# Kernel tuning notes

Hardware: AMD Instinct MI355X
Metric: run time of the kernel (lower is better)

## Reference

```python
import jax, jax.numpy as jnp
import numpy as np

SEQ, BATCH, D_IN, D_LAT = 512, 64, 1024, 1024

def setup_inputs() -> dict:
    key = jax.random.key(0)
    ks = jax.random.split(key, 5)
    scale = 0.02
    d_cat = D_IN + D_LAT
    return {
        "x":   jax.random.normal(ks[0], (SEQ, BATCH, D_IN), dtype=jnp.float32),
        "W_f": jax.random.normal(ks[1], (D_LAT, d_cat), dtype=jnp.float32) * scale,
        "b_f": jnp.zeros((D_LAT,), dtype=jnp.float32),
        "W_i": jax.random.normal(ks[2], (D_LAT, d_cat), dtype=jnp.float32) * scale,
        "b_i": jnp.zeros((D_LAT,), dtype=jnp.float32),
        "W_o": jax.random.normal(ks[3], (D_LAT, d_cat), dtype=jnp.float32) * scale,
        "b_o": jnp.zeros((D_LAT,), dtype=jnp.float32),
        "W_c": jax.random.normal(ks[4], (D_LAT, d_cat), dtype=jnp.float32) * scale,
        "b_c": jnp.zeros((D_LAT,), dtype=jnp.float32),
    }

def reference(x, W_f, b_f, W_i, b_i, W_o, b_o, W_c, b_c):
    # Fuse the 4 gate projections into one GEMM per step (same math).
    d_lat = W_f.shape[0]
    W_all = jnp.concatenate([W_f, W_i, W_o, W_c], axis=0)   # [4*d_lat, d_cat]
    b_all = jnp.concatenate([b_f, b_i, b_o, b_c], axis=0)   # [4*d_lat]
    batch = x.shape[1]
    h0 = jnp.zeros((batch, d_lat), dtype=x.dtype)
    c0 = jnp.zeros((batch, d_lat), dtype=x.dtype)

    def step(carry, x_t):
        h, c = carry
        z = jnp.concatenate([h, x_t], axis=-1)               # [batch, d_lat+d_in]
        gates = z @ W_all.T + b_all                          # [batch, 4*d_lat]
        f_t = jax.nn.sigmoid(gates[:, 0*d_lat:1*d_lat])
        i_t = jax.nn.sigmoid(gates[:, 1*d_lat:2*d_lat])
        o_t = jax.nn.sigmoid(gates[:, 2*d_lat:3*d_lat])
        g_t = jnp.tanh(gates[:, 3*d_lat:4*d_lat])
        c_t = f_t * c + i_t * g_t
        h_t = o_t * jnp.tanh(c_t)
        return (h_t, c_t), h_t

    _, hidden_states = jax.lax.scan(step, (h0, c0), x)       # [seq, batch, d_lat]
    return hidden_states
```

## Files before the change

### kernel.cpp

```cpp
#include <hip/hip_runtime.h>

#define SEQ   512
#define BATCH 64
#define D_IN  1024
#define D_LAT 1024
#define D_CAT 2048
#define NBLK  128
#define JPB   8
#define ROWS  32
#define THREADS 512
#define GPS   67

typedef unsigned short u16;
typedef __attribute__((ext_vector_type(8))) short short8;
typedef __attribute__((ext_vector_type(4))) float floatx4;

__device__ __forceinline__ u16 f2bf(float f) {
    union { float f; unsigned u; } a; a.f = f;
    unsigned u = a.u;
    return (u16)((u + 0x7FFFu + ((u >> 16) & 1u)) >> 16);
}

__device__ __forceinline__ float sigm(float x)  { return 1.0f / (1.0f + __expf(-x)); }
__device__ __forceinline__ float tanhf_(float x){ return 2.0f / (1.0f + __expf(-2.0f * x)) - 1.0f; }

__global__ void cvt_bf16(const float* __restrict__ x, u16* __restrict__ xb, int n8) {
    int i = blockIdx.x * blockDim.x + threadIdx.x;
    int stride = gridDim.x * blockDim.x;
    for (; i < n8; i += stride) {
        float4 v0 = ((const float4*)x)[2 * i];
        float4 v1 = ((const float4*)x)[2 * i + 1];
        short8 o;
        o[0] = (short)f2bf(v0.x); o[1] = (short)f2bf(v0.y);
        o[2] = (short)f2bf(v0.z); o[3] = (short)f2bf(v0.w);
        o[4] = (short)f2bf(v1.x); o[5] = (short)f2bf(v1.y);
        o[6] = (short)f2bf(v1.z); o[7] = (short)f2bf(v1.w);
        *(short8*)(xb + 8 * (size_t)i) = o;
    }
}


__launch_bounds__(THREADS, 1)
__global__ void lstm_persist(const float* __restrict__ Wf, const float* __restrict__ bfp,
                             const float* __restrict__ Wi, const float* __restrict__ bip,
                             const float* __restrict__ Wo, const float* __restrict__ bop,
                             const float* __restrict__ Wc, const float* __restrict__ bcp,
                             const u16* __restrict__ xb,
                             u16* __restrict__ hhist,
                             float* __restrict__ out,
                             unsigned* __restrict__ bar) {
    __shared__ __align__(16) float gp[8][ROWS][GPS];
    __shared__ float biasL[ROWS];

    const int tid  = threadIdx.x;
    const int jblk = blockIdx.x;
    const int c    = tid >> 6;
    const int lane = tid & 63;
    const int m    = lane & 15;
    const int q    = lane >> 4;
    const int grp  = jblk & 7;

    short8 bregH[2][4], bregX[2][4];
    #pragma unroll
    for (int rt = 0; rt < 2; ++rt) {
        const int rr  = rt * 16 + m;
        const int g   = rr >> 3;
        const int jj2 = rr & 7;
        const float* Wg = (g == 0) ? Wf : (g == 1) ? Wi : (g == 2) ? Wo : Wc;
        const float* rowp = Wg + (size_t)(jblk * JPB + jj2) * D_CAT;
        #pragma unroll
        for (int ks = 0; ks < 4; ++ks) {
            const float* ph = rowp + c * 128 + ks * 32 + q * 8;
            const float* px = rowp + 1024 + c * 128 + ks * 32 + q * 8;
            float4 h0 = *(const float4*)(ph);
            float4 h1 = *(const float4*)(ph + 4);
            float4 x0 = *(const float4*)(px);
            float4 x1 = *(const float4*)(px + 4);
            short8 bh, bx;
            bh[0] = (short)f2bf(h0.x); bh[1] = (short)f2bf(h0.y);
            bh[2] = (short)f2bf(h0.z); bh[3] = (short)f2bf(h0.w);
            bh[4] = (short)f2bf(h1.x); bh[5] = (short)f2bf(h1.y);
            bh[6] = (short)f2bf(h1.z); bh[7] = (short)f2bf(h1.w);
            bx[0] = (short)f2bf(x0.x); bx[1] = (short)f2bf(x0.y);
            bx[2] = (short)f2bf(x0.z); bx[3] = (short)f2bf(x0.w);
            bx[4] = (short)f2bf(x1.x); bx[5] = (short)f2bf(x1.y);
            bx[6] = (short)f2bf(x1.z); bx[7] = (short)f2bf(x1.w);
            bregH[rt][ks] = bh;
            bregX[rt][ks] = bx;
        }
    }
    if (tid < ROWS) {
        const float* bsrc = (tid < 8) ? bfp : (tid < 16) ? bip : (tid < 24) ? bop : bcp;
        biasL[tid] = bsrc[jblk * JPB + (tid & 7)];
    }
    __syncthreads();

    const int cb = tid >> 2;
    const int ca = tid & 3;
    float creg0 = 0.0f, creg1 = 0.0f;

    const int colbase = c * 128 + q * 8;

    #pragma unroll 1
    for (int t = 0; t < SEQ; ++t) {
        const u16* xptr = xb + (size_t)t * (BATCH * D_IN) + colbase;

        floatx4 acc[2][4];
        #pragma unroll
        for (int rt = 0; rt < 2; ++rt)
            #pragma unroll
            for (int bt = 0; bt < 4; ++bt)
                acc[rt][bt] = (floatx4){0.f, 0.f, 0.f, 0.f};

        #pragma unroll
        for (int ks = 0; ks < 4; ++ks) {
            #pragma unroll
            for (int bt = 0; bt < 4; ++bt) {
                short8 a = *(const short8*)(xptr + (size_t)(bt * 16 + m) * 1024 + ks * 32);
                acc[0][bt] = __builtin_amdgcn_mfma_f32_16x16x32_bf16(a, bregX[0][ks], acc[0][bt], 0, 0, 0);
                acc[1][bt] = __builtin_amdgcn_mfma_f32_16x16x32_bf16(a, bregX[1][ks], acc[1][bt], 0, 0, 0);
            }
        }

        asm volatile("" ::: "memory");
        if (tid == 0) {
            while (__hip_atomic_load(&bar[16], __ATOMIC_RELAXED,
                                     __HIP_MEMORY_SCOPE_AGENT) < (unsigned)t) {
                __builtin_amdgcn_s_sleep(2);
            }
        }
        __syncthreads();
        asm volatile("" ::: "memory");

        const u16* hptr = hhist + (size_t)t * (BATCH * D_LAT) + colbase;
        #pragma unroll
        for (int ks = 0; ks < 4; ++ks) {
            #pragma unroll
            for (int bt = 0; bt < 4; ++bt) {
                short8 a = *(const short8*)(hptr + (size_t)(bt * 16 + m) * 1024 + ks * 32);
                acc[0][bt] = __builtin_amdgcn_mfma_f32_16x16x32_bf16(a, bregH[0][ks], acc[0][bt], 0, 0, 0);
                acc[1][bt] = __builtin_amdgcn_mfma_f32_16x16x32_bf16(a, bregH[1][ks], acc[1][bt], 0, 0, 0);
            }
        }

        #pragma unroll
        for (int rt = 0; rt < 2; ++rt)
            #pragma unroll
            for (int bt = 0; bt < 4; ++bt)
                #pragma unroll
                for (int r = 0; r < 4; ++r)
                    gp[c][rt * 16 + m][bt * 16 + q * 4 + r] = acc[rt][bt][r];
        __syncthreads();

        if (tid < 256) {
            float h0, h1;
            {
                const int jj = 2 * ca;
                float pf = biasL[jj], pi = biasL[8 + jj], po = biasL[16 + jj], pg = biasL[24 + jj];
                #pragma unroll
                for (int cc = 0; cc < 8; ++cc) {
                    pf += gp[cc][jj][cb];
                    pi += gp[cc][8 + jj][cb];
                    po += gp[cc][16 + jj][cb];
                    pg += gp[cc][24 + jj][cb];
                }
                float ft = sigm(pf), it = sigm(pi), ot = sigm(po), gt = tanhf_(pg);
                creg0 = ft * creg0 + it * gt;
                h0 = ot * tanhf_(creg0);
            }
            {
                const int jj = 2 * ca + 1;
                float pf = biasL[jj], pi = biasL[8 + jj], po = biasL[16 + jj], pg = biasL[24 + jj];
                #pragma unroll
                for (int cc = 0; cc < 8; ++cc) {
                    pf += gp[cc][jj][cb];
                    pi += gp[cc][8 + jj][cb];
                    po += gp[cc][16 + jj][cb];
                    pg += gp[cc][24 + jj][cb];
                }
                float ft = sigm(pf), it = sigm(pi), ot = sigm(po), gt = tanhf_(pg);
                creg1 = ft * creg1 + it * gt;
                h1 = ot * tanhf_(creg1);
            }
            const int jglob = jblk * JPB + 2 * ca;
            unsigned hv = (unsigned)f2bf(h0) | ((unsigned)f2bf(h1) << 16);
            unsigned* hp = (unsigned*)(hhist + (size_t)(t + 1) * (BATCH * D_LAT)
                                             + (size_t)cb * D_LAT + jglob);
            __hip_atomic_store(hp, hv, __ATOMIC_RELAXED, __HIP_MEMORY_SCOPE_AGENT);
            float2 ov = make_float2(h0, h1);
            *(float2*)(out + (size_t)t * (BATCH * D_LAT) + (size_t)cb * D_LAT + jglob) = ov;
        }

        __syncthreads();

        if (tid == 0) {
            unsigned pg = __hip_atomic_fetch_add(&bar[32 + 16 * grp], 1u, __ATOMIC_RELAXED,
                                                 __HIP_MEMORY_SCOPE_AGENT);
            if (pg == (unsigned)(t + 1) * (NBLK / 8) - 1u) {
                unsigned pa = __hip_atomic_fetch_add(&bar[0], 1u, __ATOMIC_RELAXED,
                                                     __HIP_MEMORY_SCOPE_AGENT);
                if (pa == (unsigned)(t + 1) * 8u - 1u) {
                    __hip_atomic_store(&bar[16], (unsigned)(t + 1), __ATOMIC_RELAXED,
                                       __HIP_MEMORY_SCOPE_AGENT);
                }
            }
        }
        asm volatile("" ::: "memory");
    }
}

extern "C" void kernel_launch(void* const* d_in, const int* in_sizes, int n_in,
                              void* d_out, int out_size, void* d_ws, size_t ws_size,
                              hipStream_t stream) {
    const float* x  = (const float*)d_in[0];
    const float* Wf = (const float*)d_in[1];
    const float* bf = (const float*)d_in[2];
    const float* Wi = (const float*)d_in[3];
    const float* bi = (const float*)d_in[4];
    const float* Wo = (const float*)d_in[5];
    const float* bo = (const float*)d_in[6];
    const float* Wc = (const float*)d_in[7];
    const float* bc = (const float*)d_in[8];
    float* out = (float*)d_out;

    char* ws = (char*)d_ws;
    unsigned* bar = (unsigned*)ws;
    u16* hhist = (u16*)(ws + 1024);
    u16* xb    = (u16*)(ws + 1024 + (size_t)(SEQ + 1) * BATCH * D_LAT * 2);

    hipMemsetAsync(ws, 0, 1024 + (size_t)BATCH * D_LAT * 2, stream);
    cvt_bf16<<<2048, 256, 0, stream>>>(x, xb, SEQ * BATCH * D_IN / 8);
    lstm_persist<<<NBLK, THREADS, 0, stream>>>(Wf, bf, Wi, bi, Wo, bo, Wc, bc,
                                               xb, hhist, out, bar);
}
```

Measured before the change: 4.898 ms.

## Replace hierarchical grid barrier with per-block flags and warp-specialized x-projection prefetch

Replaces the two-level atomic counter barrier with per-block ready slots that each warp polls only for the 16 producer blocks whose h columns it reads, so a warp can start as soon as its dependencies finish. Warps 0-3 now handle the gate epilogue while warps 4-7 compute the next step's input projection (x part) during that time, taking it off the critical path. It also raises launch bounds to 2 and clears wdone via a workgroup-scope counter. The risks are register pressure from the larger bregX, the ordering of relaxed atomics with only s_waitcnt, and extra polling traffic.

```diff
diff --git a/kernel.cpp b/kernel.cpp
--- a/kernel.cpp
+++ b/kernel.cpp
@@ -40,7 +40,7 @@
 }
 
 
-__launch_bounds__(THREADS, 1)
+__launch_bounds__(THREADS, 2)
 __global__ void lstm_persist(const float* __restrict__ Wf, const float* __restrict__ bfp,
                              const float* __restrict__ Wi, const float* __restrict__ bip,
                              const float* __restrict__ Wo, const float* __restrict__ bop,
@@ -48,9 +48,10 @@
                              const u16* __restrict__ xb,
                              u16* __restrict__ hhist,
                              float* __restrict__ out,
-                             unsigned* __restrict__ bar) {
+                             unsigned* __restrict__ slots) {
     __shared__ __align__(16) float gp[8][ROWS][GPS];
     __shared__ float biasL[ROWS];
+    __shared__ unsigned wdone;
 
     const int tid  = threadIdx.x;
     const int jblk = blockIdx.x;
@@ -58,9 +59,11 @@
     const int lane = tid & 63;
     const int m    = lane & 15;
     const int q    = lane >> 4;
-    const int grp  = jblk & 7;
-
-    short8 bregH[2][4], bregX[2][4];
+
+    if (tid == 0) wdone = 0u;
+
+    short8 bregH[2][4];
+    short8 bregX[2][8];
     #pragma unroll
     for (int rt = 0; rt < 2; ++rt) {
         const int rr  = rt * 16 + m;
@@ -71,22 +74,28 @@
         #pragma unroll
         for (int ks = 0; ks < 4; ++ks) {
             const float* ph = rowp + c * 128 + ks * 32 + q * 8;
-            const float* px = rowp + 1024 + c * 128 + ks * 32 + q * 8;
             float4 h0 = *(const float4*)(ph);
             float4 h1 = *(const float4*)(ph + 4);
-            float4 x0 = *(const float4*)(px);
-            float4 x1 = *(const float4*)(px + 4);
-            short8 bh, bx;
+            short8 bh;
             bh[0] = (short)f2bf(h0.x); bh[1] = (short)f2bf(h0.y);
             bh[2] = (short)f2bf(h0.z); bh[3] = (short)f2bf(h0.w);
             bh[4] = (short)f2bf(h1.x); bh[5] = (short)f2bf(h1.y);
             bh[6] = (short)f2bf(h1.z); bh[7] = (short)f2bf(h1.w);
-            bx[0] = (short)f2bf(x0.x); bx[1] = (short)f2bf(x0.y);
-            bx[2] = (short)f2bf(x0.z); bx[3] = (short)f2bf(x0.w);
-            bx[4] = (short)f2bf(x1.x); bx[5] = (short)f2bf(x1.y);
-            bx[6] = (short)f2bf(x1.z); bx[7] = (short)f2bf(x1.w);
             bregH[rt][ks] = bh;
-            bregX[rt][ks] = bx;
+        }
+        if (c >= 4) {
+            #pragma unroll
+            for (int ks = 0; ks < 8; ++ks) {
+                const float* px = rowp + 1024 + (c - 4) * 256 + ks * 32 + q * 8;
+                float4 x0 = *(const float4*)(px);
+                float4 x1 = *(const float4*)(px + 4);
+                short8 bx;
+                bx[0] = (short)f2bf(x0.x); bx[1] = (short)f2bf(x0.y);
+                bx[2] = (short)f2bf(x0.z); bx[3] = (short)f2bf(x0.w);
+                bx[4] = (short)f2bf(x1.x); bx[5] = (short)f2bf(x1.y);
+                bx[6] = (short)f2bf(x1.z); bx[7] = (short)f2bf(x1.w);
+                bregX[rt][ks] = bx;
+            }
         }
     }
     if (tid < ROWS) {
@@ -99,49 +108,46 @@
     const int ca = tid & 3;
     float creg0 = 0.0f, creg1 = 0.0f;
 
-    const int colbase = c * 128 + q * 8;
-
-    #pragma unroll 1
-    for (int t = 0; t < SEQ; ++t) {
-        const u16* xptr = xb + (size_t)t * (BATCH * D_IN) + colbase;
-
-        floatx4 acc[2][4];
-        #pragma unroll
-        for (int rt = 0; rt < 2; ++rt)
-            #pragma unroll
-            for (int bt = 0; bt < 4; ++bt)
-                acc[rt][bt] = (floatx4){0.f, 0.f, 0.f, 0.f};
-
-        #pragma unroll
-        for (int ks = 0; ks < 4; ++ks) {
+    floatx4 acc[2][4];
+    #pragma unroll
+    for (int rt = 0; rt < 2; ++rt)
+        #pragma unroll
+        for (int bt = 0; bt < 4; ++bt)
+            acc[rt][bt] = (floatx4){0.f, 0.f, 0.f, 0.f};
+
+    if (c >= 4) {
+        const u16* xptr = xb + (size_t)(c - 4) * 256 + q * 8;
+        #pragma unroll
+        for (int ks = 0; ks < 8; ++ks)
             #pragma unroll
             for (int bt = 0; bt < 4; ++bt) {
                 short8 a = *(const short8*)(xptr + (size_t)(bt * 16 + m) * 1024 + ks * 32);
                 acc[0][bt] = __builtin_amdgcn_mfma_f32_16x16x32_bf16(a, bregX[0][ks], acc[0][bt], 0, 0, 0);
                 acc[1][bt] = __builtin_amdgcn_mfma_f32_16x16x32_bf16(a, bregX[1][ks], acc[1][bt], 0, 0, 0);
             }
-        }
-
+    }
+
+    const unsigned* myslot = slots + 16 * c + (lane & 15);
+
+    #pragma unroll 1
+    for (int t = 0; t < SEQ; ++t) {
+        for (;;) {
+            unsigned v = __hip_atomic_load(myslot, __ATOMIC_RELAXED,
+                                           __HIP_MEMORY_SCOPE_AGENT);
+            if (__all((int)(v >= (unsigned)t))) break;
+            __builtin_amdgcn_s_sleep(1);
+        }
         asm volatile("" ::: "memory");
-        if (tid == 0) {
-            while (__hip_atomic_load(&bar[16], __ATOMIC_RELAXED,
-                                     __HIP_MEMORY_SCOPE_AGENT) < (unsigned)t) {
-                __builtin_amdgcn_s_sleep(2);
-            }
-        }
-        __syncthreads();
-        asm volatile("" ::: "memory");
-
-        const u16* hptr = hhist + (size_t)t * (BATCH * D_LAT) + colbase;
-        #pragma unroll
-        for (int ks = 0; ks < 4; ++ks) {
+
+        const u16* hptr = hhist + (size_t)t * (BATCH * D_LAT) + c * 128 + q * 8;
+        #pragma unroll
+        for (int ks = 0; ks < 4; ++ks)
             #pragma unroll
             for (int bt = 0; bt < 4; ++bt) {
                 short8 a = *(const short8*)(hptr + (size_t)(bt * 16 + m) * 1024 + ks * 32);
                 acc[0][bt] = __builtin_amdgcn_mfma_f32_16x16x32_bf16(a, bregH[0][ks], acc[0][bt], 0, 0, 0);
                 acc[1][bt] = __builtin_amdgcn_mfma_f32_16x16x32_bf16(a, bregH[1][ks], acc[1][bt], 0, 0, 0);
             }
-        }
 
         #pragma unroll
         for (int rt = 0; rt < 2; ++rt)
@@ -189,23 +195,41 @@
             __hip_atomic_store(hp, hv, __ATOMIC_RELAXED, __HIP_MEMORY_SCOPE_AGENT);
             float2 ov = make_float2(h0, h1);
             *(float2*)(out + (size_t)t * (BATCH * D_LAT) + (size_t)cb * D_LAT + jglob) = ov;
+
+            asm volatile("s_waitcnt vmcnt(0)" ::: "memory");
+            if (lane == 0) {
+                unsigned old = __hip_atomic_fetch_add(&wdone, 1u, __ATOMIC_RELAXED,
+                                                      __HIP_MEMORY_SCOPE_WORKGROUP);
+                if (old == 4u * (unsigned)t + 3u) {
+                    __hip_atomic_store(&slots[jblk], (unsigned)(t + 1),
+                                       __ATOMIC_RELAXED, __HIP_MEMORY_SCOPE_AGENT);
+                }
+            }
+            #pragma unroll
+            for (int rt = 0; rt < 2; ++rt)
+                #pragma unroll
+                for (int bt = 0; bt < 4; ++bt)
+                    acc[rt][bt] = (floatx4){0.f, 0.f, 0.f, 0.f};
+        } else {
+            #pragma unroll
+            for (int rt = 0; rt < 2; ++rt)
+                #pragma unroll
+                for (int bt = 0; bt < 4; ++bt)
+                    acc[rt][bt] = (floatx4){0.f, 0.f, 0.f, 0.f};
+            if (t + 1 < SEQ) {
+                const u16* xptr = xb + (size_t)(t + 1) * (BATCH * D_IN) + (c - 4) * 256 + q * 8;
+                #pragma unroll
+                for (int ks = 0; ks < 8; ++ks)
+                    #pragma unroll
+                    for (int bt = 0; bt < 4; ++bt) {
+                        short8 a = *(const short8*)(xptr + (size_t)(bt * 16 + m) * 1024 + ks * 32);
+                        acc[0][bt] = __builtin_amdgcn_mfma_f32_16x16x32_bf16(a, bregX[0][ks], acc[0][bt], 0, 0, 0);
+                        acc[1][bt] = __builtin_amdgcn_mfma_f32_16x16x32_bf16(a, bregX[1][ks], acc[1][bt], 0, 0, 0);
+                    }
+            }
         }
 
         __syncthreads();
-
-        if (tid == 0) {
-            unsigned pg = __hip_atomic_fetch_add(&bar[32 + 16 * grp], 1u, __ATOMIC_RELAXED,
-                                                 __HIP_MEMORY_SCOPE_AGENT);
-            if (pg == (unsigned)(t + 1) * (NBLK / 8) - 1u) {
-                unsigned pa = __hip_atomic_fetch_add(&bar[0], 1u, __ATOMIC_RELAXED,
-                                                     __HIP_MEMORY_SCOPE_AGENT);
-                if (pa == (unsigned)(t + 1) * 8u - 1u) {
-                    __hip_atomic_store(&bar[16], (unsigned)(t + 1), __ATOMIC_RELAXED,
-                                       __HIP_MEMORY_SCOPE_AGENT);
-                }
-            }
-        }
-        asm volatile("" ::: "memory");
     }
 }
 
@@ -224,12 +248,12 @@
     float* out = (float*)d_out;
 
     char* ws = (char*)d_ws;
-    unsigned* bar = (unsigned*)ws;
+    unsigned* slots = (unsigned*)ws;
     u16* hhist = (u16*)(ws + 1024);
     u16* xb    = (u16*)(ws + 1024 + (size_t)(SEQ + 1) * BATCH * D_LAT * 2);
 
     hipMemsetAsync(ws, 0, 1024 + (size_t)BATCH * D_LAT * 2, stream);
     cvt_bf16<<<2048, 256, 0, stream>>>(x, xb, SEQ * BATCH * D_IN / 8);
     lstm_persist<<<NBLK, THREADS, 0, stream>>>(Wf, bf, Wi, bi, Wo, bo, Wc, bc,
-                                               xb, hhist, out, bar);
-}
+                                               xb, hhist, out, slots);
+}
```

Result: no change. 4.908 ms (+0.2%).
